# Kernel tuning notes

Measured on AMD Instinct MI355X. Metric: run time of the kernel, lower is better.

Reference implementation:

```python
import jax, jax.numpy as jnp
import numpy as np

D_MODEL = 1024
NUM_HEADS = 16
HEAD_DIM = D_MODEL // NUM_HEADS


def setup_inputs() -> dict:
    key = jax.random.key(0)
    ks = jax.random.split(key, 9)
    B, T = 2, 2048
    s = 1.0 / np.sqrt(D_MODEL)
    return {
        "x": jax.random.normal(ks[0], (B, T, D_MODEL), dtype=jnp.float32),
        "Wq": jax.random.normal(ks[1], (D_MODEL, D_MODEL), dtype=jnp.float32) * s,
        "bq": jnp.zeros((D_MODEL,), dtype=jnp.float32),
        "Wk": jax.random.normal(ks[2], (D_MODEL, D_MODEL), dtype=jnp.float32) * s,
        "bk": jnp.zeros((D_MODEL,), dtype=jnp.float32),
        "Wv": jax.random.normal(ks[3], (D_MODEL, D_MODEL), dtype=jnp.float32) * s,
        "bv": jnp.zeros((D_MODEL,), dtype=jnp.float32),
        "Wo": jax.random.normal(ks[4], (D_MODEL, D_MODEL), dtype=jnp.float32) * s,
        "bo": jnp.zeros((D_MODEL,), dtype=jnp.float32),
    }


def reference(x, Wq, bq, Wk, bk, Wv, bv, Wo, bo):
    B, T, D = x.shape
    H, Hd = NUM_HEADS, HEAD_DIM
    # Linear projections; weights stored as [in, out] (torch Linear transposed)
    q = (x @ Wq + bq).reshape(B, T, H, Hd)
    k = (x @ Wk + bk).reshape(B, T, H, Hd)
    v = (x @ Wv + bv).reshape(B, T, H, Hd)
    scale = 1.0 / jnp.sqrt(jnp.asarray(Hd, dtype=x.dtype))
    scores = jnp.einsum("bqhd,bkhd->bhqk", q, k) * scale  # [B,H,T,T]
    attn = jax.nn.softmax(scores, axis=-1)
    ctx = jnp.einsum("bhqk,bkhd->bqhd", attn, v).reshape(B, T, D)
    return ctx @ Wo + bo
```

## Files before the change

### kernel.cpp

```cpp
#include <hip/hip_runtime.h>


typedef unsigned short ushort_t;
typedef __attribute__((ext_vector_type(8))) short bf16x8;
typedef __attribute__((ext_vector_type(4))) short bf16x4;
typedef __attribute__((ext_vector_type(4))) float f32x4;

#define BATCH 2
#define SEQ   2048
#define DM    1024
#define NH    16
#define HD    64
#define MTOT  (BATCH*SEQ)

#if __has_builtin(__builtin_amdgcn_exp2f)
#define EXP2(x) __builtin_amdgcn_exp2f(x)
#else
#define EXP2(x) exp2f(x)
#endif

__device__ __forceinline__ ushort_t f2bf(float f) {
    union { float f; unsigned int u; } v; v.f = f;
    unsigned int r = v.u + 0x7fffu + ((v.u >> 16) & 1u);
    return (ushort_t)(r >> 16);
}

__device__ __forceinline__ void gload_lds16(const void* g, void* l) {
    __builtin_amdgcn_global_load_lds(
        (const __attribute__((address_space(1))) unsigned int*)g,
        (__attribute__((address_space(3))) unsigned int*)l, 16, 0, 0);
}

__global__ __launch_bounds__(256) void prep_kernel(const float* __restrict__ x,
                                                   const float* __restrict__ W0,
                                                   const float* __restrict__ W1,
                                                   const float* __restrict__ W2,
                                                   const float* __restrict__ W3,
                                                   ushort_t* __restrict__ xb,
                                                   ushort_t* __restrict__ Wtb) {
    __shared__ ushort_t tile[64][72];
    int bid = blockIdx.x, tid = threadIdx.x;
    if (bid < 4096) {
        int i = bid * 256 + tid;
        float4 v = ((const float4*)x)[i];
        ushort4 o;
        o.x = f2bf(v.x); o.y = f2bf(v.y); o.z = f2bf(v.z); o.w = f2bf(v.w);
        ((ushort4*)xb)[i] = o;
        return;
    }
    int b2 = bid - 4096;
    const float* Ws[4] = {W0, W1, W2, W3};
    const float* W = Ws[b2 >> 8];
    ushort_t* Wt = Wtb + (size_t)(b2 >> 8) * DM * DM;
    int k0 = ((b2 >> 4) & 15) * 64, n0 = (b2 & 15) * 64;
    int tr = tid >> 4;
    int tc = (tid & 15) * 4;
#pragma unroll
    for (int j = 0; j < 4; j++) {
        int r = j * 16 + tr;
        float4 v = *(const float4*)&W[(size_t)(k0 + r) * DM + n0 + tc];
        tile[r][tc + 0] = f2bf(v.x); tile[r][tc + 1] = f2bf(v.y);
        tile[r][tc + 2] = f2bf(v.z); tile[r][tc + 3] = f2bf(v.w);
    }
    __syncthreads();
#pragma unroll
    for (int j = 0; j < 4; j++) {
        int n = j * 16 + tr;
        ushort4 o;
        o.x = tile[tc + 0][n]; o.y = tile[tc + 1][n];
        o.z = tile[tc + 2][n]; o.w = tile[tc + 3][n];
        *(ushort4*)&Wt[(size_t)(n0 + n) * DM + k0 + tc] = o;
    }
}

__global__ __launch_bounds__(256) void gemm_qkv(const ushort_t* __restrict__ A,
                                                const ushort_t* __restrict__ Wtb,
                                                const float* __restrict__ bq,
                                                const float* __restrict__ bk,
                                                const float* __restrict__ bv,
                                                ushort_t* __restrict__ qo,
                                                ushort_t* __restrict__ ko,
                                                ushort_t* __restrict__ vo) {
    __shared__ ushort_t As[2][128 * 32];
    __shared__ ushort_t Bs[2][128 * 32];
    int sel = blockIdx.x >> 3;
    const ushort_t* Wt = Wtb + (size_t)sel * DM * DM;
    const float* bias = sel == 0 ? bq : (sel == 1 ? bk : bv);
    int tid = threadIdx.x;
    int w = tid >> 6, lane = tid & 63, lr = lane & 15, lg = lane >> 4;
    int wr = w >> 1, wc = w & 1;
    int m0 = blockIdx.y * 128, n0 = (blockIdx.x & 7) * 128;

    int srow = (w * 2) * 16 + (lane >> 2);
    int scb = (lane & 3) * 8;
    const ushort_t* ag = &A[(size_t)(m0 + srow) * DM + scb];
    const ushort_t* bg = &Wt[(size_t)(n0 + srow) * DM + scb];
    int ldst = (w * 2) * 1024;

    f32x4 acc[4][4] = {};

#pragma unroll
    for (int p = 0; p < 2; p++) {
        gload_lds16(ag + (size_t)p * 16 * DM, (char*)As[0] + ldst + p * 1024);
        gload_lds16(bg + (size_t)p * 16 * DM, (char*)Bs[0] + ldst + p * 1024);
    }
    __syncthreads();

    for (int kt = 0; kt < 32; ++kt) {
        int cur = kt & 1;
        if (kt + 1 < 32) {
            int k0 = (kt + 1) << 5;
#pragma unroll
            for (int p = 0; p < 2; p++) {
                gload_lds16(ag + (size_t)p * 16 * DM + k0, (char*)As[cur ^ 1] + ldst + p * 1024);
                gload_lds16(bg + (size_t)p * 16 * DM + k0, (char*)Bs[cur ^ 1] + ldst + p * 1024);
            }
        }
        bf16x8 af[4], bfr[4];
#pragma unroll
        for (int i = 0; i < 4; i++) {
            af[i]  = *(const bf16x8*)&As[cur][(wr * 64 + i * 16 + lr) * 32 + lg * 8];
            bfr[i] = *(const bf16x8*)&Bs[cur][(wc * 64 + i * 16 + lr) * 32 + lg * 8];
        }
#pragma unroll
        for (int mi = 0; mi < 4; mi++)
#pragma unroll
            for (int ni = 0; ni < 4; ni++)
                acc[mi][ni] = __builtin_amdgcn_mfma_f32_16x16x32_bf16(
                    af[mi], bfr[ni], acc[mi][ni], 0, 0, 0);
        __syncthreads();
    }

    float scale = (sel == 0) ? 0.125f * 1.44269504f : 1.0f;
#pragma unroll
    for (int mi = 0; mi < 4; mi++) {
#pragma unroll
        for (int ni = 0; ni < 4; ni++) {
            f32x4 a = acc[mi][ni];
            int n = n0 + wc * 64 + ni * 16 + lr;
            float bs = bias[n];
            int mbase = m0 + wr * 64 + mi * 16 + lg * 4;
            int hh = n >> 6, d = n & 63;
            if (sel == 2) {
                int b = mbase >> 11, tt = mbase & 2047;
                size_t base = ((size_t)(b * NH + hh) * HD + d) * SEQ + tt;
                ushort4 pk;
                pk.x = f2bf(a[0] + bs); pk.y = f2bf(a[1] + bs);
                pk.z = f2bf(a[2] + bs); pk.w = f2bf(a[3] + bs);
                *(ushort4*)&vo[base] = pk;
            } else {
                ushort_t* o = sel ? ko : qo;
#pragma unroll
                for (int r = 0; r < 4; r++) {
                    int m = mbase + r;
                    int b = m >> 11, tt = m & 2047;
                    o[((size_t)(b * NH + hh) * SEQ + tt) * HD + d] =
                        f2bf((a[r] + bs) * scale);
                }
            }
        }
    }
}

__global__ __launch_bounds__(256) void gemm_out(const ushort_t* __restrict__ A,
                                                const ushort_t* __restrict__ Wt,
                                                const float* __restrict__ bias,
                                                float* __restrict__ out) {
    __shared__ ushort_t As[2][128 * 32];
    __shared__ ushort_t Bs[2][128 * 32];
    int tid = threadIdx.x;
    int w = tid >> 6, lane = tid & 63, lr = lane & 15, lg = lane >> 4;
    int wr = w >> 1, wc = w & 1;
    int m0 = blockIdx.y * 128, n0 = blockIdx.x * 128;

    int srow = (w * 2) * 16 + (lane >> 2);
    int scb = (lane & 3) * 8;
    const ushort_t* ag = &A[(size_t)(m0 + srow) * DM + scb];
    const ushort_t* bg = &Wt[(size_t)(n0 + srow) * DM + scb];
    int ldst = (w * 2) * 1024;

    f32x4 acc[4][4] = {};

#pragma unroll
    for (int p = 0; p < 2; p++) {
        gload_lds16(ag + (size_t)p * 16 * DM, (char*)As[0] + ldst + p * 1024);
        gload_lds16(bg + (size_t)p * 16 * DM, (char*)Bs[0] + ldst + p * 1024);
    }
    __syncthreads();

    for (int kt = 0; kt < 32; ++kt) {
        int cur = kt & 1;
        if (kt + 1 < 32) {
            int k0 = (kt + 1) << 5;
#pragma unroll
            for (int p = 0; p < 2; p++) {
                gload_lds16(ag + (size_t)p * 16 * DM + k0, (char*)As[cur ^ 1] + ldst + p * 1024);
                gload_lds16(bg + (size_t)p * 16 * DM + k0, (char*)Bs[cur ^ 1] + ldst + p * 1024);
            }
        }
        bf16x8 af[4], bfr[4];
#pragma unroll
        for (int i = 0; i < 4; i++) {
            af[i]  = *(const bf16x8*)&As[cur][(wr * 64 + i * 16 + lr) * 32 + lg * 8];
            bfr[i] = *(const bf16x8*)&Bs[cur][(wc * 64 + i * 16 + lr) * 32 + lg * 8];
        }
#pragma unroll
        for (int mi = 0; mi < 4; mi++)
#pragma unroll
            for (int ni = 0; ni < 4; ni++)
                acc[mi][ni] = __builtin_amdgcn_mfma_f32_16x16x32_bf16(
                    af[mi], bfr[ni], acc[mi][ni], 0, 0, 0);
        __syncthreads();
    }

#pragma unroll
    for (int mi = 0; mi < 4; mi++) {
#pragma unroll
        for (int ni = 0; ni < 4; ni++) {
            f32x4 a = acc[mi][ni];
            int n = n0 + wc * 64 + ni * 16 + lr;
            float bs = bias[n];
            int mbase = m0 + wr * 64 + mi * 16 + lg * 4;
#pragma unroll
            for (int r = 0; r < 4; r++)
                out[(size_t)(mbase + r) * DM + n] = a[r] + bs;
        }
    }
}

__device__ __forceinline__ void softmax_pack(f32x4 (&s)[8], float& l_run,
                                             int4 (&pwv)[4]) {
    float rs0 = 0.f, rs1 = 0.f, rs2 = 0.f, rs3 = 0.f;
#pragma unroll
    for (int nt = 0; nt < 8; ++nt) {
        float p0 = EXP2(s[nt][0]);
        float p1 = EXP2(s[nt][1]);
        float p2 = EXP2(s[nt][2]);
        float p3 = EXP2(s[nt][3]);
        s[nt][0] = p0; s[nt][1] = p1; s[nt][2] = p2; s[nt][3] = p3;
        rs0 += p0; rs1 += p1; rs2 += p2; rs3 += p3;
    }
    float rs = (rs0 + rs1) + (rs2 + rs3);
    rs += __shfl_xor(rs, 16);
    rs += __shfl_xor(rs, 32);
    l_run += rs;
#pragma unroll
    for (int kk = 0; kk < 4; ++kk) {
        unsigned pw[4];
#pragma unroll
        for (int hh = 0; hh < 2; ++hh)
#pragma unroll
            for (int pr = 0; pr < 2; ++pr) {
                unsigned rr;
                asm("v_cvt_pk_bf16_f32 %0, %1, %2"
                    : "=v"(rr)
                    : "v"(s[kk + 4 * hh][2 * pr]), "v"(s[kk + 4 * hh][2 * pr + 1]));
                pw[hh * 2 + pr] = rr;
            }
        pwv[kk] = make_int4(pw[0], pw[1], pw[2], pw[3]);
    }
}

__global__ __launch_bounds__(512, 2) void attn_kernel(const ushort_t* __restrict__ Q,
                                                      const ushort_t* __restrict__ Kb,
                                                      const ushort_t* __restrict__ Vt,
                                                      ushort_t* __restrict__ Ctx) {
    __shared__ ushort_t Ks[2][128 * 64];
    __shared__ ushort_t Vs[2][64 * 128];

    int tid = threadIdx.x, w = tid >> 6, lane = tid & 63, lr = lane & 15, lg = lane >> 4;
    int orig = blockIdx.x;
    int wg = (orig & 7) * 32 + (orig >> 3);
    int qb = wg & 7, bh = wg >> 3;
    int q0 = qb * 256;

    const ushort_t* Qp = Q + (size_t)bh * SEQ * HD;
    const ushort_t* Kp = Kb + (size_t)bh * SEQ * HD;
    const ushort_t* Vp = Vt + (size_t)bh * HD * SEQ;

    int qrow = q0 + w * 16 + lr;
    bf16x8 aqA[2], aqB[2];
    aqA[0] = *(const bf16x8*)&Qp[(size_t)qrow * HD + lg * 8];
    aqA[1] = *(const bf16x8*)&Qp[(size_t)qrow * HD + 32 + lg * 8];
    aqB[0] = *(const bf16x8*)&Qp[(size_t)(qrow + 128) * HD + lg * 8];
    aqB[1] = *(const bf16x8*)&Qp[(size_t)(qrow + 128) * HD + 32 + lg * 8];

    f32x4 oaccA[4] = {}, oaccB[4] = {};
    float lA = 0.f, lB = 0.f;

    int krow = tid >> 3, kch = tid & 7;
    int kbyte = krow * 128 + ((kch * 16) ^ ((krow & 7) << 4));
    const ushort_t* kg0 = &Kp[(size_t)krow * HD + kch * 8];
    const ushort_t* kg1 = &Kp[(size_t)(krow + 64) * HD + kch * 8];
    int vrow = tid >> 4, vch = tid & 15;
    int S_a2 = (((vch >> 1) & 3) * 32 + (vch & 1) * 16 + (vch >> 3) * 4) * 2;
    int vswz = (vrow & 7) << 4;
    int vbyte0 = vrow * 256 + (S_a2 ^ vswz);
    int vbyte1 = vrow * 256 + ((S_a2 + 16) ^ vswz);
    const ushort_t* vg0 = &Vp[(size_t)vrow * SEQ + vch * 8];
    const ushort_t* vg1 = &Vp[(size_t)(vrow + 32) * SEQ + vch * 8];

    {
        bf16x8 k0v = *(const bf16x8*)kg0;
        bf16x8 k1v = *(const bf16x8*)kg1;
        bf16x8 v0v = *(const bf16x8*)vg0;
        bf16x8 v1v = *(const bf16x8*)vg1;
        *(bf16x8*)((char*)Ks[0] + kbyte) = k0v;
        *(bf16x8*)((char*)Ks[0] + kbyte + 64 * 128) = k1v;
        union { bf16x8 v; bf16x4 h[2]; } u0, u1;
        u0.v = v0v; u1.v = v1v;
        *(bf16x4*)((char*)Vs[0] + vbyte0) = u0.h[0];
        *(bf16x4*)((char*)Vs[0] + vbyte1) = u0.h[1];
        *(bf16x4*)((char*)Vs[0] + vbyte0 + 32 * 256) = u1.h[0];
        *(bf16x4*)((char*)Vs[0] + vbyte1 + 32 * 256) = u1.h[1];
    }
    __syncthreads();

    int kread = lr * 128;
    int kswz = (lr & 7) << 4;

    for (int t = 0; t < SEQ / 128; ++t) {
        int cur = t & 1;
        bf16x8 kr0, kr1, vr0, vr1;
        bool more = (t + 1 < SEQ / 128);
        if (more) {
            size_t ko_off = (size_t)(t + 1) * 128 * HD;
            int vo_off = (t + 1) * 128;
            kr0 = *(const bf16x8*)(kg0 + ko_off);
            kr1 = *(const bf16x8*)(kg1 + ko_off);
            vr0 = *(const bf16x8*)(vg0 + vo_off);
            vr1 = *(const bf16x8*)(vg1 + vo_off);
        }

        f32x4 sA[8], sB[8];
        __builtin_amdgcn_s_setprio(1);
#pragma unroll
        for (int nt = 0; nt < 8; ++nt) {
            f32x4 a = {}, b = {};
#pragma unroll
            for (int kk = 0; kk < 2; ++kk) {
                bf16x8 bk = *(const bf16x8*)((char*)Ks[cur] + nt * 2048 + kread +
                                             ((kk * 64 + lg * 16) ^ kswz));
                a = __builtin_amdgcn_mfma_f32_16x16x32_bf16(bk, aqA[kk], a, 0, 0, 0);
                b = __builtin_amdgcn_mfma_f32_16x16x32_bf16(bk, aqB[kk], b, 0, 0, 0);
            }
            sA[nt] = a; sB[nt] = b;
        }
        __builtin_amdgcn_s_setprio(0);

        int4 pwvA[4], pwvB[4];
        softmax_pack(sA, lA, pwvA);
        softmax_pack(sB, lB, pwvB);

        __builtin_amdgcn_s_setprio(1);
#pragma unroll
        for (int dt = 0; dt < 4; ++dt) {
            int vbase = (dt * 16 + lr) * 256;
#pragma unroll
            for (int kk = 0; kk < 4; ++kk) {
                bf16x8 bv = *(const bf16x8*)((char*)Vs[cur] + vbase +
                                             ((kk * 64 + lg * 16) ^ kswz));
                oaccA[dt] = __builtin_amdgcn_mfma_f32_16x16x32_bf16(
                    *(bf16x8*)&pwvA[kk], bv, oaccA[dt], 0, 0, 0);
                oaccB[dt] = __builtin_amdgcn_mfma_f32_16x16x32_bf16(
                    *(bf16x8*)&pwvB[kk], bv, oaccB[dt], 0, 0, 0);
            }
        }
        __builtin_amdgcn_s_setprio(0);

        if (more) {
            char* kd = (char*)Ks[cur ^ 1];
            char* vd = (char*)Vs[cur ^ 1];
            *(bf16x8*)(kd + kbyte) = kr0;
            *(bf16x8*)(kd + kbyte + 64 * 128) = kr1;
            union { bf16x8 v; bf16x4 h[2]; } u0, u1;
            u0.v = vr0; u1.v = vr1;
            *(bf16x4*)(vd + vbyte0) = u0.h[0];
            *(bf16x4*)(vd + vbyte1) = u0.h[1];
            *(bf16x4*)(vd + vbyte0 + 32 * 256) = u1.h[0];
            *(bf16x4*)(vd + vbyte1 + 32 * 256) = u1.h[1];
            __syncthreads();
        }
    }

    float invA = 1.0f / lA, invB = 1.0f / lB;
    float ivA[4], ivB[4];
#pragma unroll
    for (int r = 0; r < 4; ++r) {
        ivA[r] = __shfl(invA, lg * 4 + r);
        ivB[r] = __shfl(invB, lg * 4 + r);
    }
    int b = bh >> 4, h = bh & 15;
#pragma unroll
    for (int dt = 0; dt < 4; ++dt)
#pragma unroll
        for (int r = 0; r < 4; ++r) {
            int q = q0 + w * 16 + lg * 4 + r;
            Ctx[((size_t)(b * SEQ + q)) * DM + h * HD + dt * 16 + lr] =
                f2bf(oaccA[dt][r] * ivA[r]);
            Ctx[((size_t)(b * SEQ + q + 128)) * DM + h * HD + dt * 16 + lr] =
                f2bf(oaccB[dt][r] * ivB[r]);
        }
}

extern "C" void kernel_launch(void* const* d_in, const int* in_sizes, int n_in,
                              void* d_out, int out_size, void* d_ws, size_t ws_size,
                              hipStream_t stream) {
    const float* x  = (const float*)d_in[0];
    const float* Wq = (const float*)d_in[1];
    const float* bq = (const float*)d_in[2];
    const float* Wk = (const float*)d_in[3];
    const float* bk = (const float*)d_in[4];
    const float* Wv = (const float*)d_in[5];
    const float* bv = (const float*)d_in[6];
    const float* Wo = (const float*)d_in[7];
    const float* bo = (const float*)d_in[8];
    float* out = (float*)d_out;

    ushort_t* xbf = (ushort_t*)d_ws;
    ushort_t* wtb = xbf + (size_t)MTOT * DM;
    ushort_t* qbf = wtb + (size_t)4 * DM * DM;
    ushort_t* kbf = qbf + (size_t)MTOT * DM;
    ushort_t* vtb = kbf + (size_t)MTOT * DM;
    ushort_t* ctx = vtb + (size_t)MTOT * DM;

    prep_kernel<<<4096 + 1024, 256, 0, stream>>>(x, Wq, Wk, Wv, Wo, xbf, wtb);

    gemm_qkv<<<dim3(24, 32), 256, 0, stream>>>(xbf, wtb, bq, bk, bv, qbf, kbf, vtb);

    attn_kernel<<<256, 512, 0, stream>>>(qbf, kbf, vtb, ctx);

    gemm_out<<<dim3(8, 32), 256, 0, stream>>>(ctx, wtb + (size_t)3 * DM * DM, bo, out);
}
```

Baseline: 123.3 us.

## Triple-buffer LDS in projection GEMMs with one barrier per k-step

Both projection GEMMs move from double to triple LDS buffering. Each k-step now issues the next tile's direct-to-LDS loads, waits only on the older outstanding loads with a partial vmcnt, and hits a single raw s_barrier, replacing the two __syncthreads per iteration. The third buffer means the tile being overwritten is never the one other waves may still be reading, so the trailing barrier can go and loads overlap compute. In exchange LDS per block grows by half, which can lower occupancy, and correctness now depends on hand-written waitcnt counts matching the compiler's load issue.

Measured after the change: 119.0 us (median of 2 runs). -3.4%, faster.

```diff
diff --git a/kernel.cpp b/kernel.cpp
--- a/kernel.cpp
+++ b/kernel.cpp
@@ -81,8 +81,8 @@
                                                 ushort_t* __restrict__ qo,
                                                 ushort_t* __restrict__ ko,
                                                 ushort_t* __restrict__ vo) {
-    __shared__ ushort_t As[2][128 * 32];
-    __shared__ ushort_t Bs[2][128 * 32];
+    __shared__ ushort_t As[3][128 * 32];
+    __shared__ ushort_t Bs[3][128 * 32];
     int sel = blockIdx.x >> 3;
     const ushort_t* Wt = Wtb + (size_t)sel * DM * DM;
     const float* bias = sel == 0 ? bq : (sel == 1 ? bk : bv);
@@ -104,18 +104,26 @@
         gload_lds16(ag + (size_t)p * 16 * DM, (char*)As[0] + ldst + p * 1024);
         gload_lds16(bg + (size_t)p * 16 * DM, (char*)Bs[0] + ldst + p * 1024);
     }
-    __syncthreads();
-
+
+    int cur = 0;
     for (int kt = 0; kt < 32; ++kt) {
-        int cur = kt & 1;
         if (kt + 1 < 32) {
+            int nxt = cur + 1 == 3 ? 0 : cur + 1;
             int k0 = (kt + 1) << 5;
 #pragma unroll
             for (int p = 0; p < 2; p++) {
-                gload_lds16(ag + (size_t)p * 16 * DM + k0, (char*)As[cur ^ 1] + ldst + p * 1024);
-                gload_lds16(bg + (size_t)p * 16 * DM + k0, (char*)Bs[cur ^ 1] + ldst + p * 1024);
-            }
-        }
+                gload_lds16(ag + (size_t)p * 16 * DM + k0, (char*)As[nxt] + ldst + p * 1024);
+                gload_lds16(bg + (size_t)p * 16 * DM + k0, (char*)Bs[nxt] + ldst + p * 1024);
+            }
+            __builtin_amdgcn_sched_barrier(0);
+            asm volatile("s_waitcnt vmcnt(4)" ::: "memory");
+        } else {
+            __builtin_amdgcn_sched_barrier(0);
+            asm volatile("s_waitcnt vmcnt(0)" ::: "memory");
+        }
+        __builtin_amdgcn_s_barrier();
+        __builtin_amdgcn_sched_barrier(0);
+
         bf16x8 af[4], bfr[4];
 #pragma unroll
         for (int i = 0; i < 4; i++) {
@@ -128,7 +136,7 @@
             for (int ni = 0; ni < 4; ni++)
                 acc[mi][ni] = __builtin_amdgcn_mfma_f32_16x16x32_bf16(
                     af[mi], bfr[ni], acc[mi][ni], 0, 0, 0);
-        __syncthreads();
+        cur = cur + 1 == 3 ? 0 : cur + 1;
     }
 
     float scale = (sel == 0) ? 0.125f * 1.44269504f : 1.0f;
@@ -166,8 +174,8 @@
                                                 const ushort_t* __restrict__ Wt,
                                                 const float* __restrict__ bias,
                                                 float* __restrict__ out) {
-    __shared__ ushort_t As[2][128 * 32];
-    __shared__ ushort_t Bs[2][128 * 32];
+    __shared__ ushort_t As[3][128 * 32];
+    __shared__ ushort_t Bs[3][128 * 32];
     int tid = threadIdx.x;
     int w = tid >> 6, lane = tid & 63, lr = lane & 15, lg = lane >> 4;
     int wr = w >> 1, wc = w & 1;
@@ -186,18 +194,26 @@
         gload_lds16(ag + (size_t)p * 16 * DM, (char*)As[0] + ldst + p * 1024);
         gload_lds16(bg + (size_t)p * 16 * DM, (char*)Bs[0] + ldst + p * 1024);
     }
-    __syncthreads();
-
+
+    int cur = 0;
     for (int kt = 0; kt < 32; ++kt) {
-        int cur = kt & 1;
         if (kt + 1 < 32) {
+            int nxt = cur + 1 == 3 ? 0 : cur + 1;
             int k0 = (kt + 1) << 5;
 #pragma unroll
             for (int p = 0; p < 2; p++) {
-                gload_lds16(ag + (size_t)p * 16 * DM + k0, (char*)As[cur ^ 1] + ldst + p * 1024);
-                gload_lds16(bg + (size_t)p * 16 * DM + k0, (char*)Bs[cur ^ 1] + ldst + p * 1024);
-            }
-        }
+                gload_lds16(ag + (size_t)p * 16 * DM + k0, (char*)As[nxt] + ldst + p * 1024);
+                gload_lds16(bg + (size_t)p * 16 * DM + k0, (char*)Bs[nxt] + ldst + p * 1024);
+            }
+            __builtin_amdgcn_sched_barrier(0);
+            asm volatile("s_waitcnt vmcnt(4)" ::: "memory");
+        } else {
+            __builtin_amdgcn_sched_barrier(0);
+            asm volatile("s_waitcnt vmcnt(0)" ::: "memory");
+        }
+        __builtin_amdgcn_s_barrier();
+        __builtin_amdgcn_sched_barrier(0);
+
         bf16x8 af[4], bfr[4];
 #pragma unroll
         for (int i = 0; i < 4; i++) {
@@ -210,7 +226,7 @@
             for (int ni = 0; ni < 4; ni++)
                 acc[mi][ni] = __builtin_amdgcn_mfma_f32_16x16x32_bf16(
                     af[mi], bfr[ni], acc[mi][ni], 0, 0, 0);
-        __syncthreads();
+        cur = cur + 1 == 3 ? 0 : cur + 1;
     }
 
 #pragma unroll
```
